# Optimization experiments

Measured on AMD Instinct MI355X. Metric: run time of the kernel, lower is better.

Reference implementation:

```python
import jax, jax.numpy as jnp
import numpy as np

PAD_IDX = 0


def setup_inputs() -> dict:
    key = jax.random.key(0)
    ks = jax.random.split(key, 6)
    nentries, entry_size, bsize, nemb, vocab = 8000, 32, 64, 256, 50000
    keys = jax.random.randint(ks[0], (nentries,), 0, vocab)
    entries = jax.random.randint(ks[1], (nentries, entry_size), 0, vocab)
    query = jax.random.normal(ks[2], (bsize, nemb), dtype=jnp.float32)
    wordemb = jax.random.normal(ks[3], (vocab, nemb), dtype=jnp.float32)
    qproj_w = jax.random.uniform(ks[4], (nemb, nemb), jnp.float32, -0.1, 0.1)
    qproj_b = jnp.zeros((nemb,), jnp.float32)
    return dict(keys=keys, entries=entries, query=query, wordemb=wordemb,
                qproj_w=qproj_w, qproj_b=qproj_b)


def _embed(ids, wordemb):
    # F.embedding with padding_idx: gathered rows at pad_idx are zeroed
    return wordemb[ids] * (ids != PAD_IDX)[..., None].astype(wordemb.dtype)


def reference(keys, entries, query, wordemb, qproj_w, qproj_b):
    keys_e = _embed(keys, wordemb)       # (m, d)
    ents_e = _embed(entries, wordemb)    # (m, n, d)
    # --- single hop (max_hops = 1) ---
    # value_atten: query attends over the n tokens inside each entry
    vq = query @ qproj_w.T + qproj_b                       # (b, d)
    logits_v = jnp.einsum('ik,mnk->imn', vq, ents_e)       # (b, m, n)
    prob_v = jax.nn.softmax(logits_v, axis=-1)
    ents = jnp.einsum('imn,mnk->imk', prob_v, ents_e)      # (b, m, d)
    # entry_atten: query attends over entries via their keys
    logits_e = jnp.einsum('ik,jk->ij', query, keys_e)      # (b, m)
    prob_e = jax.nn.softmax(logits_e, axis=-1)
    o_k = prob_e @ keys_e                                  # (b, d)
    combined = jnp.einsum('bm,bme->be', prob_e, ents)      # (b, d)
    # return (us[-1], prob_list[-1], combined_entries)
    return o_k, logits_e, combined
```

## Files before the change

kernel.cpp:

```cpp
#include <hip/hip_runtime.h>
#include <math.h>

#define B 64
#define D 256
#define M 8000
#define N 32
#define LG_LD 8000
#define EPB 16
#define NBLK (M / EPB)

typedef unsigned short u16;
typedef __bf16 bf16x8 __attribute__((ext_vector_type(8)));
typedef float fx4 __attribute__((ext_vector_type(4)));

#define STR_E  264
#define STR_P  40

static __device__ __forceinline__ u16 f2bf(float x) {
    unsigned int u = __float_as_uint(x);
    u += 0x7FFFu + ((u >> 16) & 1u);
    return (u16)(u >> 16);
}
static __device__ __forceinline__ float bf2f(u16 h) {
    return __uint_as_float(((unsigned)h) << 16);
}
static __device__ __forceinline__ uint4 pack8(float4 va, float4 vb, float msk) {
    unsigned p0 = (unsigned)f2bf(va.x * msk) | ((unsigned)f2bf(va.y * msk) << 16);
    unsigned p1 = (unsigned)f2bf(va.z * msk) | ((unsigned)f2bf(va.w * msk) << 16);
    unsigned p2 = (unsigned)f2bf(vb.x * msk) | ((unsigned)f2bf(vb.y * msk) << 16);
    unsigned p3 = (unsigned)f2bf(vb.z * msk) | ((unsigned)f2bf(vb.w * msk) << 16);
    return make_uint4(p0, p1, p2, p3);
}

__global__ __launch_bounds__(256) void k_prep2(const int* __restrict__ keys,
                                               const float* __restrict__ emb,
                                               const float* __restrict__ q,
                                               const float* __restrict__ W,
                                               const float* __restrict__ bias,
                                               u16* __restrict__ qbf,
                                               u16* __restrict__ keb,
                                               u16* __restrict__ vqb) {
    __shared__ float qs[D];
    int t = threadIdx.x, bid = blockIdx.x;
    if (bid < 1000) {
        int c = bid * 256 + t;
        int j = c >> 5, sp = c & 31;
        int id = keys[j];
        const float* rp = emb + (size_t)id * D + sp * 8;
        float4 v0 = *(const float4*)rp;
        float4 v1 = *(const float4*)(rp + 4);
        float msk = (id != 0) ? 1.f : 0.f;
        uint4 pk = pack8(v0, v1, msk);
        *(uint4*)(keb + (size_t)j * D + sp * 8) = pk;
    } else if (bid < 1008) {
        size_t idx = (size_t)(bid - 1000) * 2048 + (size_t)t * 8;
        float4 v0 = *(const float4*)(q + idx);
        float4 v1 = *(const float4*)(q + idx + 4);
        uint4 pk = pack8(v0, v1, 1.f);
        *(uint4*)(qbf + idx) = pk;
    } else {
        int b = bid - 1008;
        qs[t] = q[b * D + t];
        __syncthreads();
        const float* wr = W + t * D;
        float acc = bias[t];
#pragma unroll 8
        for (int k = 0; k < D; k += 4) {
            float4 w4 = *(const float4*)(wr + k);
            acc += qs[k] * w4.x + qs[k + 1] * w4.y + qs[k + 2] * w4.z + qs[k + 3] * w4.w;
        }
        vqb[b * D + t] = f2bf(acc);
    }
}

__global__ __launch_bounds__(256, 2) void k_heavy_f(const int* __restrict__ entries,
                                                    const float* __restrict__ emb,
                                                    const u16* __restrict__ vqb,
                                                    const u16* __restrict__ qbf,
                                                    const u16* __restrict__ keb,
                                                    float* __restrict__ lg,
                                                    u16* __restrict__ numCp,
                                                    u16* __restrict__ numKp,
                                                    float* __restrict__ mLp,
                                                    float* __restrict__ denLp) {
    __shared__ __align__(16) u16 sEu[2][N * STR_E];
    __shared__ __align__(16) u16 sETu[2][64 * 136];
    __shared__ __align__(16) u16 sPu[B * STR_P];
    __shared__ float sw[EPB][B];

    int t = threadIdx.x;
    int lane = t & 63, l = lane & 15, q = lane >> 4, w = t >> 6;
    int b0 = 16 * w;
    int sp = t & 31, n0 = t >> 5;
    int m0 = blockIdx.x * EPB;
    int bb = t & 63, y = t >> 6;

    int idc[4], idn[4];
    float4 pfF[8];
#pragma unroll
    for (int i = 0; i < 4; ++i) idc[i] = entries[m0 * N + n0 + 8 * i];
#pragma unroll
    for (int i = 0; i < 4; ++i) {
        const float* rp = emb + (size_t)idc[i] * D + sp * 8;
        pfF[2 * i]     = *(const float4*)rp;
        pfF[2 * i + 1] = *(const float4*)(rp + 4);
    }

    fx4 zero4 = {0.f, 0.f, 0.f, 0.f};
    fx4 aL = zero4;
#pragma unroll
    for (int s = 0; s < 8; ++s) {
        bf16x8 a  = *(const bf16x8*)(qbf + (size_t)(b0 + l) * D + 32 * s + 8 * q);
        bf16x8 bq = *(const bf16x8*)(keb + (size_t)(m0 + l) * D + 32 * s + 8 * q);
        aL = __builtin_amdgcn_mfma_f32_16x16x32_bf16(a, bq, aL, 0, 0, 0);
    }
#pragma unroll
    for (int r = 0; r < 4; ++r)
        lg[(size_t)(b0 + 4 * q + r) * LG_LD + m0 + l] = aL[r];

#pragma unroll
    for (int r = 0; r < 4; ++r) {
        float m_ = aL[r];
        m_ = fmaxf(m_, __shfl_xor(m_, 1));
        m_ = fmaxf(m_, __shfl_xor(m_, 2));
        m_ = fmaxf(m_, __shfl_xor(m_, 4));
        m_ = fmaxf(m_, __shfl_xor(m_, 8));
        float wv = __expf(aL[r] - m_);
        sw[l][b0 + 4 * q + r] = wv;
        float d_ = wv;
        d_ += __shfl_xor(d_, 1);
        d_ += __shfl_xor(d_, 2);
        d_ += __shfl_xor(d_, 4);
        d_ += __shfl_xor(d_, 8);
        if (l == 0) {
            mLp[blockIdx.x * B + b0 + 4 * q + r] = m_;
            denLp[blockIdx.x * B + b0 + 4 * q + r] = d_;
        }
    }

    bf16x8 vqf[8];
#pragma unroll
    for (int s = 0; s < 8; ++s)
        vqf[s] = *(const bf16x8*)(vqb + (b0 + l) * D + 32 * s + 8 * q);

    fx4 acc[16];
#pragma unroll
    for (int dt = 0; dt < 16; ++dt) acc[dt] = zero4;

    {
        uint4 pk[4];
#pragma unroll
        for (int i = 0; i < 4; ++i) {
            float msk = (idc[i] != 0) ? 1.f : 0.f;
            pk[i] = pack8(pfF[2 * i], pfF[2 * i + 1], msk);
            *(uint4*)&sEu[0][(n0 + 8 * i) * STR_E + sp * 8] = pk[i];
        }
#pragma unroll
        for (int j = 0; j < 8; ++j) {
            unsigned a0 = (((unsigned*)&pk[0])[j >> 1] >> ((j & 1) * 16)) & 0xFFFFu;
            unsigned a1 = (((unsigned*)&pk[1])[j >> 1] >> ((j & 1) * 16)) & 0xFFFFu;
            unsigned a2 = (((unsigned*)&pk[2])[j >> 1] >> ((j & 1) * 16)) & 0xFFFFu;
            unsigned a3 = (((unsigned*)&pk[3])[j >> 1] >> ((j & 1) * 16)) & 0xFFFFu;
            uint2 pr = make_uint2(a0 | (a1 << 16), a2 | (a3 << 16));
            int off = (2 * sp + (j >> 2)) * 136 + (n0 >> 1) * 32 + (j & 3) * 8 + (n0 & 1) * 4;
            *(uint2*)&sETu[0][off] = pr;
        }
    }
#pragma unroll
    for (int i = 0; i < 4; ++i) idc[i] = entries[(m0 + 1) * N + n0 + 8 * i];
#pragma unroll
    for (int i = 0; i < 4; ++i) {
        const float* rp = emb + (size_t)idc[i] * D + sp * 8;
        pfF[2 * i]     = *(const float4*)rp;
        pfF[2 * i + 1] = *(const float4*)(rp + 4);
    }
#pragma unroll
    for (int i = 0; i < 4; ++i) idn[i] = entries[(m0 + 2) * N + n0 + 8 * i];

    int offL = (l >> 2) * 136 + (l & 3) * 8;

#pragma unroll 2
    for (int e = 0; e < EPB; ++e) {
        __syncthreads();
        int nxt = (e + 1) & 1;
        if (e < EPB - 1) {
            uint4 pk[4];
#pragma unroll
            for (int i = 0; i < 4; ++i) {
                float msk = (idc[i] != 0) ? 1.f : 0.f;
                pk[i] = pack8(pfF[2 * i], pfF[2 * i + 1], msk);
                *(uint4*)&sEu[nxt][(n0 + 8 * i) * STR_E + sp * 8] = pk[i];
            }
#pragma unroll
            for (int j = 0; j < 8; ++j) {
                unsigned a0 = (((unsigned*)&pk[0])[j >> 1] >> ((j & 1) * 16)) & 0xFFFFu;
                unsigned a1 = (((unsigned*)&pk[1])[j >> 1] >> ((j & 1) * 16)) & 0xFFFFu;
                unsigned a2 = (((unsigned*)&pk[2])[j >> 1] >> ((j & 1) * 16)) & 0xFFFFu;
                unsigned a3 = (((unsigned*)&pk[3])[j >> 1] >> ((j & 1) * 16)) & 0xFFFFu;
                uint2 pr = make_uint2(a0 | (a1 << 16), a2 | (a3 << 16));
                int off = (2 * sp + (j >> 2)) * 136 + (n0 >> 1) * 32 + (j & 3) * 8 + (n0 & 1) * 4;
                *(uint2*)&sETu[nxt][off] = pr;
            }
            if (e < EPB - 2) {
#pragma unroll
                for (int i = 0; i < 4; ++i) {
                    const float* rp = emb + (size_t)idn[i] * D + sp * 8;
                    pfF[2 * i]     = *(const float4*)rp;
                    pfF[2 * i + 1] = *(const float4*)(rp + 4);
                }
#pragma unroll
                for (int i = 0; i < 4; ++i) idc[i] = idn[i];
                if (e < EPB - 3) {
#pragma unroll
                    for (int i = 0; i < 4; ++i) idn[i] = entries[(m0 + e + 3) * N + n0 + 8 * i];
                }
            }
        }
        int cur = e & 1;
        fx4 accS[2];
        accS[0] = zero4; accS[1] = zero4;
#pragma unroll
        for (int T = 0; T < 2; ++T)
#pragma unroll
            for (int s = 0; s < 8; ++s) {
                bf16x8 ea = *(const bf16x8*)&sEu[cur][(16 * T + l) * STR_E + 32 * s + 8 * q];
                accS[T] = __builtin_amdgcn_mfma_f32_16x16x32_bf16(ea, vqf[s], accS[T], 0, 0, 0);
            }
        float swb = sw[e][b0 + l];
        float mx = -INFINITY;
#pragma unroll
        for (int T = 0; T < 2; ++T)
#pragma unroll
            for (int r = 0; r < 4; ++r) mx = fmaxf(mx, accS[T][r]);
        mx = fmaxf(mx, __shfl_xor(mx, 16));
        mx = fmaxf(mx, __shfl_xor(mx, 32));
        float pe[2][4], sum = 0.f;
#pragma unroll
        for (int T = 0; T < 2; ++T)
#pragma unroll
            for (int r = 0; r < 4; ++r) {
                pe[T][r] = __expf(accS[T][r] - mx);
                sum += pe[T][r];
            }
        sum += __shfl_xor(sum, 16);
        sum += __shfl_xor(sum, 32);
        float sc = swb / sum;
#pragma unroll
        for (int T = 0; T < 2; ++T)
#pragma unroll
            for (int r = 0; r < 4; ++r) {
                int nn = 16 * T + 4 * q + r;
                int slot = 4 * (nn & 7) + (nn >> 3);
                sPu[(b0 + l) * STR_P + slot] = f2bf(pe[T][r] * sc);
            }
        bf16x8 pa = *(const bf16x8*)&sPu[(b0 + l) * STR_P + 8 * q];
#pragma unroll
        for (int dt = 0; dt < 16; ++dt) {
            bf16x8 eb = *(const bf16x8*)&sETu[cur][offL + dt * 544 + q * 32];
            acc[dt] = __builtin_amdgcn_mfma_f32_16x16x32_bf16(pa, eb, acc[dt], 0, 0, 0);
        }
    }

    u16* ncp = numCp + (size_t)blockIdx.x * (B * D);
#pragma unroll
    for (int dt = 0; dt < 16; ++dt)
#pragma unroll
        for (int r = 0; r < 4; ++r)
            ncp[(b0 + 4 * q + r) * D + 16 * dt + l] = f2bf(acc[dt][r]);

    __syncthreads();
    {
        int rp = t >> 5;
        uint4 ka = *(const uint4*)(keb + (size_t)(m0 + rp) * D + sp * 8);
        uint4 kb = *(const uint4*)(keb + (size_t)(m0 + rp + 8) * D + sp * 8);
#pragma unroll
        for (int j = 0; j < 8; ++j) {
            unsigned a0 = (((unsigned*)&ka)[j >> 1] >> ((j & 1) * 16)) & 0xFFFFu;
            unsigned a1 = (((unsigned*)&kb)[j >> 1] >> ((j & 1) * 16)) & 0xFFFFu;
            int d = 8 * sp + j;
            int sl = 2 * rp;
            int off = (d >> 2) * 136 + (sl >> 3) * 32 + (d & 3) * 8 + (sl & 7);
            *(unsigned*)&sETu[0][off] = a0 | (a1 << 16);
        }
#pragma unroll
        for (int i = 0; i < 4; ++i) {
            int m = 4 * i + y;
            int slot = 2 * (m & 7) + (m >> 3);
            sPu[bb * STR_P + slot] = f2bf(sw[m][bb]);
        }
        *(uint2*)&sPu[bb * STR_P + 16 + 4 * y] = make_uint2(0u, 0u);
    }
    __syncthreads();
    fx4 acc2[16];
#pragma unroll
    for (int dt = 0; dt < 16; ++dt) acc2[dt] = zero4;
    {
        bf16x8 pa2 = *(const bf16x8*)&sPu[(b0 + l) * STR_P + 8 * q];
#pragma unroll
        for (int dt = 0; dt < 16; ++dt) {
            bf16x8 eb2 = *(const bf16x8*)&sETu[0][offL + dt * 544 + q * 32];
            acc2[dt] = __builtin_amdgcn_mfma_f32_16x16x32_bf16(pa2, eb2, acc2[dt], 0, 0, 0);
        }
    }
    u16* nkp = numKp + (size_t)blockIdx.x * (B * D);
#pragma unroll
    for (int dt = 0; dt < 16; ++dt)
#pragma unroll
        for (int r = 0; r < 4; ++r)
            nkp[(b0 + 4 * q + r) * D + 16 * dt + l] = f2bf(acc2[dt][r]);
}

__global__ __launch_bounds__(256) void k_comb2(const u16* __restrict__ numCp,
                                               const u16* __restrict__ numKp,
                                               const float* __restrict__ mLp,
                                               const float* __restrict__ denLp,
                                               float* __restrict__ o_k,
                                               float* __restrict__ comb) {
    __shared__ float sscale[NBLK];
    __shared__ float red[256];
    __shared__ float ro[8][32], rc[8][32];
    __shared__ float srden;
    int bid = blockIdx.x;
    int b = bid >> 3, d0 = (bid & 7) * 32;
    int t = threadIdx.x;
    float mx = -INFINITY;
    for (int blk = t; blk < NBLK; blk += 256) mx = fmaxf(mx, mLp[blk * B + b]);
    red[t] = mx;
    __syncthreads();
    for (int s = 128; s > 0; s >>= 1) {
        if (t < s) red[t] = fmaxf(red[t], red[t + s]);
        __syncthreads();
    }
    float Mg = red[0];
    __syncthreads();
    float ds = 0.f;
    for (int blk = t; blk < NBLK; blk += 256) {
        float sc = __expf(mLp[blk * B + b] - Mg);
        sscale[blk] = sc;
        ds += sc * denLp[blk * B + b];
    }
    red[t] = ds;
    __syncthreads();
    for (int s = 128; s > 0; s >>= 1) {
        if (t < s) red[t] += red[t + s];
        __syncthreads();
    }
    if (t == 0) srden = 1.f / red[0];
    __syncthreads();
    int dd = t & 31, s = t >> 5;
    float ao = 0.f, ac = 0.f;
    for (int blk = s; blk < NBLK; blk += 8) {
        float sc = sscale[blk];
        size_t i = (size_t)blk * (B * D) + (size_t)b * D + d0 + dd;
        ao += sc * bf2f(numKp[i]);
        ac += sc * bf2f(numCp[i]);
    }
    ro[s][dd] = ao;
    rc[s][dd] = ac;
    __syncthreads();
    if (t < 32) {
        float so = 0.f, sc2 = 0.f;
#pragma unroll
        for (int k = 0; k < 8; ++k) { so += ro[k][t]; sc2 += rc[k][t]; }
        float rd = srden;
        o_k[b * D + d0 + t] = so * rd;
        comb[b * D + d0 + t] = sc2 * rd;
    }
}


extern "C" void kernel_launch(void* const* d_in, const int* in_sizes, int n_in,
                              void* d_out, int out_size, void* d_ws, size_t ws_size,
                              hipStream_t stream) {
    const int*   keys    = (const int*)d_in[0];
    const int*   entries = (const int*)d_in[1];
    const float* query   = (const float*)d_in[2];
    const float* wordemb = (const float*)d_in[3];
    const float* qproj_w = (const float*)d_in[4];
    const float* qproj_b = (const float*)d_in[5];

    float* out  = (float*)d_out;
    float* o_k  = out;
    float* lg   = out + B * D;
    float* comb = out + B * D + B * M;

    char* wsb = (char*)d_ws;
    u16*   keb   = (u16*)wsb;
    u16*   qbf   = (u16*)(wsb + 4096000);
    u16*   vqb   = (u16*)(wsb + 4128768);
    u16*   numCp = (u16*)(wsb + 4161536);
    u16*   numKp = (u16*)(wsb + 20545536);
    float* mLp   = (float*)(wsb + 36929536);
    float* denLp = (float*)(wsb + 37057536);

    k_prep2<<<1072, 256, 0, stream>>>(keys, wordemb, query, qproj_w, qproj_b,
                                      qbf, keb, vqb);
    k_heavy_f<<<NBLK, 256, 0, stream>>>(entries, wordemb, vqb, qbf, keb, lg,
                                        numCp, numKp, mLp, denLp);
    k_comb2<<<512, 256, 0, stream>>>(numCp, numKp, mLp, denLp, o_k, comb);
}
```

Measured before the change: 176.3 us.

## Deepen embedding gather prefetch to two entries with ping-pong register buffers

The per-entry loop now keeps two register prefetch buffers (pfA/pfB), so embedding gathers for entry e+2 are issued while entry e is computed. Before, the lookahead was one entry. The __syncthreads calls become a custom barrier that waits only on lgkmcnt, so outstanding global loads no longer stall at each barrier. The softmax-weight shared array is transposed with a padded stride to change its LDS access pattern. The cost is higher register pressure (16 float4 of prefetch state) at 2 blocks per CU, which risks spills or lower occupancy.

```diff
diff --git a/kernel.cpp b/kernel.cpp
--- a/kernel.cpp
+++ b/kernel.cpp
@@ -15,6 +15,7 @@
 
 #define STR_E  264
 #define STR_P  40
+#define STR_W  19
 
 static __device__ __forceinline__ u16 f2bf(float x) {
     unsigned int u = __float_as_uint(x);
@@ -73,6 +74,102 @@
     }
 }
 
+#define BARRIER_LGKM() do {                                   \
+    asm volatile("s_waitcnt lgkmcnt(0)" ::: "memory");        \
+    __builtin_amdgcn_s_barrier();                             \
+    asm volatile("" ::: "memory");                            \
+} while (0)
+
+#define STAGE_BODY(EE, PF, ID) do {                                                     \
+    int nxt_ = (EE) & 1;                                                                \
+    uint4 pk_[4];                                                                       \
+    _Pragma("unroll")                                                                   \
+    for (int i_ = 0; i_ < 4; ++i_) {                                                    \
+        float msk_ = ((ID)[i_] != 0) ? 1.f : 0.f;                                       \
+        pk_[i_] = pack8((PF)[2 * i_], (PF)[2 * i_ + 1], msk_);                          \
+        *(uint4*)&sEu[nxt_][(n0 + 8 * i_) * STR_E + sp * 8] = pk_[i_];                  \
+    }                                                                                   \
+    _Pragma("unroll")                                                                   \
+    for (int j_ = 0; j_ < 8; ++j_) {                                                    \
+        unsigned a0_ = (((unsigned*)&pk_[0])[j_ >> 1] >> ((j_ & 1) * 16)) & 0xFFFFu;    \
+        unsigned a1_ = (((unsigned*)&pk_[1])[j_ >> 1] >> ((j_ & 1) * 16)) & 0xFFFFu;    \
+        unsigned a2_ = (((unsigned*)&pk_[2])[j_ >> 1] >> ((j_ & 1) * 16)) & 0xFFFFu;    \
+        unsigned a3_ = (((unsigned*)&pk_[3])[j_ >> 1] >> ((j_ & 1) * 16)) & 0xFFFFu;    \
+        uint2 pr_ = make_uint2(a0_ | (a1_ << 16), a2_ | (a3_ << 16));                   \
+        int off_ = (2 * sp + (j_ >> 2)) * 136 + (n0 >> 1) * 32 + (j_ & 3) * 8 + (n0 & 1) * 4; \
+        *(uint2*)&sETu[nxt_][off_] = pr_;                                               \
+    }                                                                                   \
+} while (0)
+
+#define COMPUTE_BODY(E) do {                                                            \
+    int cur_ = (E) & 1;                                                                 \
+    fx4 accS_[2];                                                                       \
+    accS_[0] = zero4; accS_[1] = zero4;                                                 \
+    _Pragma("unroll")                                                                   \
+    for (int T_ = 0; T_ < 2; ++T_)                                                      \
+        _Pragma("unroll")                                                               \
+        for (int s_ = 0; s_ < 8; ++s_) {                                                \
+            bf16x8 ea_ = *(const bf16x8*)&sEu[cur_][(16 * T_ + l) * STR_E + 32 * s_ + 8 * q]; \
+            accS_[T_] = __builtin_amdgcn_mfma_f32_16x16x32_bf16(ea_, vqf[s_], accS_[T_], 0, 0, 0); \
+        }                                                                               \
+    float swb_ = swT[b0 + l][(E)];                                                      \
+    float mx_ = -INFINITY;                                                              \
+    _Pragma("unroll")                                                                   \
+    for (int T_ = 0; T_ < 2; ++T_)                                                      \
+        _Pragma("unroll")                                                               \
+        for (int r_ = 0; r_ < 4; ++r_) mx_ = fmaxf(mx_, accS_[T_][r_]);                 \
+    mx_ = fmaxf(mx_, __shfl_xor(mx_, 16));                                              \
+    mx_ = fmaxf(mx_, __shfl_xor(mx_, 32));                                              \
+    float pe_[2][4], sum_ = 0.f;                                                        \
+    _Pragma("unroll")                                                                   \
+    for (int T_ = 0; T_ < 2; ++T_)                                                      \
+        _Pragma("unroll")                                                               \
+        for (int r_ = 0; r_ < 4; ++r_) {                                                \
+            pe_[T_][r_] = __expf(accS_[T_][r_] - mx_);                                  \
+            sum_ += pe_[T_][r_];                                                        \
+        }                                                                               \
+    sum_ += __shfl_xor(sum_, 16);                                                       \
+    sum_ += __shfl_xor(sum_, 32);                                                       \
+    float sc_ = swb_ / sum_;                                                            \
+    _Pragma("unroll")                                                                   \
+    for (int T_ = 0; T_ < 2; ++T_)                                                      \
+        _Pragma("unroll")                                                               \
+        for (int r_ = 0; r_ < 4; ++r_) {                                                \
+            int nn_ = 16 * T_ + 4 * q + r_;                                             \
+            int slot_ = 4 * (nn_ & 7) + (nn_ >> 3);                                     \
+            sPu[(b0 + l) * STR_P + slot_] = f2bf(pe_[T_][r_] * sc_);                    \
+        }                                                                               \
+    bf16x8 pa_ = *(const bf16x8*)&sPu[(b0 + l) * STR_P + 8 * q];                        \
+    _Pragma("unroll")                                                                   \
+    for (int dt_ = 0; dt_ < 16; ++dt_) {                                                \
+        bf16x8 eb_ = *(const bf16x8*)&sETu[cur_][offL + dt_ * 544 + q * 32];            \
+        acc[dt_] = __builtin_amdgcn_mfma_f32_16x16x32_bf16(pa_, eb_, acc[dt_], 0, 0, 0); \
+    }                                                                                   \
+} while (0)
+
+#define ITER(E, PF, ID) do {                                                            \
+    BARRIER_LGKM();                                                                     \
+    if ((E) < EPB - 1) {                                                                \
+        STAGE_BODY((E) + 1, PF, ID);                                                    \
+        if ((E) < EPB - 3) {                                                            \
+            _Pragma("unroll")                                                           \
+            for (int i_ = 0; i_ < 4; ++i_) (ID)[i_] = idn[i_];                          \
+            _Pragma("unroll")                                                           \
+            for (int i_ = 0; i_ < 4; ++i_) {                                            \
+                const float* rp_ = emb + (size_t)(ID)[i_] * D + sp * 8;                 \
+                (PF)[2 * i_]     = *(const float4*)rp_;                                 \
+                (PF)[2 * i_ + 1] = *(const float4*)(rp_ + 4);                           \
+            }                                                                           \
+            if ((E) < EPB - 4) {                                                        \
+                _Pragma("unroll")                                                       \
+                for (int i_ = 0; i_ < 4; ++i_)                                          \
+                    idn[i_] = entries[(m0 + (E) + 4) * N + n0 + 8 * i_];                \
+            }                                                                           \
+        }                                                                               \
+    }                                                                                   \
+    COMPUTE_BODY(E);                                                                    \
+} while (0)
+
 __global__ __launch_bounds__(256, 2) void k_heavy_f(const int* __restrict__ entries,
                                                     const float* __restrict__ emb,
                                                     const u16* __restrict__ vqb,
@@ -86,7 +183,7 @@
     __shared__ __align__(16) u16 sEu[2][N * STR_E];
     __shared__ __align__(16) u16 sETu[2][64 * 136];
     __shared__ __align__(16) u16 sPu[B * STR_P];
-    __shared__ float sw[EPB][B];
+    __shared__ float swT[B][STR_W];
 
     int t = threadIdx.x;
     int lane = t & 63, l = lane & 15, q = lane >> 4, w = t >> 6;
@@ -95,15 +192,16 @@
     int m0 = blockIdx.x * EPB;
     int bb = t & 63, y = t >> 6;
 
-    int idc[4], idn[4];
-    float4 pfF[8];
-#pragma unroll
-    for (int i = 0; i < 4; ++i) idc[i] = entries[m0 * N + n0 + 8 * i];
+    float4 pfA[8], pfB[8];
+    int idA[4], idB[4], idn[4];
+
+#pragma unroll
+    for (int i = 0; i < 4; ++i) idB[i] = entries[m0 * N + n0 + 8 * i];
 #pragma unroll
     for (int i = 0; i < 4; ++i) {
-        const float* rp = emb + (size_t)idc[i] * D + sp * 8;
-        pfF[2 * i]     = *(const float4*)rp;
-        pfF[2 * i + 1] = *(const float4*)(rp + 4);
+        const float* rp = emb + (size_t)idB[i] * D + sp * 8;
+        pfB[2 * i]     = *(const float4*)rp;
+        pfB[2 * i + 1] = *(const float4*)(rp + 4);
     }
 
     fx4 zero4 = {0.f, 0.f, 0.f, 0.f};
@@ -126,7 +224,7 @@
         m_ = fmaxf(m_, __shfl_xor(m_, 4));
         m_ = fmaxf(m_, __shfl_xor(m_, 8));
         float wv = __expf(aL[r] - m_);
-        sw[l][b0 + 4 * q + r] = wv;
+        swT[b0 + 4 * q + r][l] = wv;
         float d_ = wv;
         d_ += __shfl_xor(d_, 1);
         d_ += __shfl_xor(d_, 2);
@@ -147,118 +245,31 @@
 #pragma unroll
     for (int dt = 0; dt < 16; ++dt) acc[dt] = zero4;
 
-    {
-        uint4 pk[4];
-#pragma unroll
-        for (int i = 0; i < 4; ++i) {
-            float msk = (idc[i] != 0) ? 1.f : 0.f;
-            pk[i] = pack8(pfF[2 * i], pfF[2 * i + 1], msk);
-            *(uint4*)&sEu[0][(n0 + 8 * i) * STR_E + sp * 8] = pk[i];
-        }
-#pragma unroll
-        for (int j = 0; j < 8; ++j) {
-            unsigned a0 = (((unsigned*)&pk[0])[j >> 1] >> ((j & 1) * 16)) & 0xFFFFu;
-            unsigned a1 = (((unsigned*)&pk[1])[j >> 1] >> ((j & 1) * 16)) & 0xFFFFu;
-            unsigned a2 = (((unsigned*)&pk[2])[j >> 1] >> ((j & 1) * 16)) & 0xFFFFu;
-            unsigned a3 = (((unsigned*)&pk[3])[j >> 1] >> ((j & 1) * 16)) & 0xFFFFu;
-            uint2 pr = make_uint2(a0 | (a1 << 16), a2 | (a3 << 16));
-            int off = (2 * sp + (j >> 2)) * 136 + (n0 >> 1) * 32 + (j & 3) * 8 + (n0 & 1) * 4;
-            *(uint2*)&sETu[0][off] = pr;
-        }
-    }
-#pragma unroll
-    for (int i = 0; i < 4; ++i) idc[i] = entries[(m0 + 1) * N + n0 + 8 * i];
+    int offL = (l >> 2) * 136 + (l & 3) * 8;
+
+    STAGE_BODY(0, pfB, idB);
+#pragma unroll
+    for (int i = 0; i < 4; ++i) idB[i] = entries[(m0 + 1) * N + n0 + 8 * i];
 #pragma unroll
     for (int i = 0; i < 4; ++i) {
-        const float* rp = emb + (size_t)idc[i] * D + sp * 8;
-        pfF[2 * i]     = *(const float4*)rp;
-        pfF[2 * i + 1] = *(const float4*)(rp + 4);
-    }
-#pragma unroll
-    for (int i = 0; i < 4; ++i) idn[i] = entries[(m0 + 2) * N + n0 + 8 * i];
-
-    int offL = (l >> 2) * 136 + (l & 3) * 8;
-
-#pragma unroll 2
-    for (int e = 0; e < EPB; ++e) {
-        __syncthreads();
-        int nxt = (e + 1) & 1;
-        if (e < EPB - 1) {
-            uint4 pk[4];
-#pragma unroll
-            for (int i = 0; i < 4; ++i) {
-                float msk = (idc[i] != 0) ? 1.f : 0.f;
-                pk[i] = pack8(pfF[2 * i], pfF[2 * i + 1], msk);
-                *(uint4*)&sEu[nxt][(n0 + 8 * i) * STR_E + sp * 8] = pk[i];
-            }
-#pragma unroll
-            for (int j = 0; j < 8; ++j) {
-                unsigned a0 = (((unsigned*)&pk[0])[j >> 1] >> ((j & 1) * 16)) & 0xFFFFu;
-                unsigned a1 = (((unsigned*)&pk[1])[j >> 1] >> ((j & 1) * 16)) & 0xFFFFu;
-                unsigned a2 = (((unsigned*)&pk[2])[j >> 1] >> ((j & 1) * 16)) & 0xFFFFu;
-                unsigned a3 = (((unsigned*)&pk[3])[j >> 1] >> ((j & 1) * 16)) & 0xFFFFu;
-                uint2 pr = make_uint2(a0 | (a1 << 16), a2 | (a3 << 16));
-                int off = (2 * sp + (j >> 2)) * 136 + (n0 >> 1) * 32 + (j & 3) * 8 + (n0 & 1) * 4;
-                *(uint2*)&sETu[nxt][off] = pr;
-            }
-            if (e < EPB - 2) {
-#pragma unroll
-                for (int i = 0; i < 4; ++i) {
-                    const float* rp = emb + (size_t)idn[i] * D + sp * 8;
-                    pfF[2 * i]     = *(const float4*)rp;
-                    pfF[2 * i + 1] = *(const float4*)(rp + 4);
-                }
-#pragma unroll
-                for (int i = 0; i < 4; ++i) idc[i] = idn[i];
-                if (e < EPB - 3) {
-#pragma unroll
-                    for (int i = 0; i < 4; ++i) idn[i] = entries[(m0 + e + 3) * N + n0 + 8 * i];
-                }
-            }
-        }
-        int cur = e & 1;
-        fx4 accS[2];
-        accS[0] = zero4; accS[1] = zero4;
-#pragma unroll
-        for (int T = 0; T < 2; ++T)
-#pragma unroll
-            for (int s = 0; s < 8; ++s) {
-                bf16x8 ea = *(const bf16x8*)&sEu[cur][(16 * T + l) * STR_E + 32 * s + 8 * q];
-                accS[T] = __builtin_amdgcn_mfma_f32_16x16x32_bf16(ea, vqf[s], accS[T], 0, 0, 0);
-            }
-        float swb = sw[e][b0 + l];
-        float mx = -INFINITY;
-#pragma unroll
-        for (int T = 0; T < 2; ++T)
-#pragma unroll
-            for (int r = 0; r < 4; ++r) mx = fmaxf(mx, accS[T][r]);
-        mx = fmaxf(mx, __shfl_xor(mx, 16));
-        mx = fmaxf(mx, __shfl_xor(mx, 32));
-        float pe[2][4], sum = 0.f;
-#pragma unroll
-        for (int T = 0; T < 2; ++T)
-#pragma unroll
-            for (int r = 0; r < 4; ++r) {
-                pe[T][r] = __expf(accS[T][r] - mx);
-                sum += pe[T][r];
-            }
-        sum += __shfl_xor(sum, 16);
-        sum += __shfl_xor(sum, 32);
-        float sc = swb / sum;
-#pragma unroll
-        for (int T = 0; T < 2; ++T)
-#pragma unroll
-            for (int r = 0; r < 4; ++r) {
-                int nn = 16 * T + 4 * q + r;
-                int slot = 4 * (nn & 7) + (nn >> 3);
-                sPu[(b0 + l) * STR_P + slot] = f2bf(pe[T][r] * sc);
-            }
-        bf16x8 pa = *(const bf16x8*)&sPu[(b0 + l) * STR_P + 8 * q];
-#pragma unroll
-        for (int dt = 0; dt < 16; ++dt) {
-            bf16x8 eb = *(const bf16x8*)&sETu[cur][offL + dt * 544 + q * 32];
-            acc[dt] = __builtin_amdgcn_mfma_f32_16x16x32_bf16(pa, eb, acc[dt], 0, 0, 0);
-        }
+        const float* rp = emb + (size_t)idB[i] * D + sp * 8;
+        pfB[2 * i]     = *(const float4*)rp;
+        pfB[2 * i + 1] = *(const float4*)(rp + 4);
+    }
+#pragma unroll
+    for (int i = 0; i < 4; ++i) idA[i] = entries[(m0 + 2) * N + n0 + 8 * i];
+#pragma unroll
+    for (int i = 0; i < 4; ++i) {
+        const float* rp = emb + (size_t)idA[i] * D + sp * 8;
+        pfA[2 * i]     = *(const float4*)rp;
+        pfA[2 * i + 1] = *(const float4*)(rp + 4);
+    }
+#pragma unroll
+    for (int i = 0; i < 4; ++i) idn[i] = entries[(m0 + 3) * N + n0 + 8 * i];
+
+    for (int e = 0; e < EPB; e += 2) {
+        ITER(e, pfB, idB);
+        ITER(e + 1, pfA, idA);
     }
 
     u16* ncp = numCp + (size_t)blockIdx.x * (B * D);
@@ -268,7 +279,7 @@
         for (int r = 0; r < 4; ++r)
             ncp[(b0 + 4 * q + r) * D + 16 * dt + l] = f2bf(acc[dt][r]);
 
-    __syncthreads();
+    BARRIER_LGKM();
     {
         int rp = t >> 5;
         uint4 ka = *(const uint4*)(keb + (size_t)(m0 + rp) * D + sp * 8);
@@ -286,11 +297,11 @@
         for (int i = 0; i < 4; ++i) {
             int m = 4 * i + y;
             int slot = 2 * (m & 7) + (m >> 3);
-            sPu[bb * STR_P + slot] = f2bf(sw[m][bb]);
+            sPu[bb * STR_P + slot] = f2bf(swT[bb][m]);
         }
         *(uint2*)&sPu[bb * STR_P + 16 + 4 * y] = make_uint2(0u, 0u);
     }
-    __syncthreads();
+    BARRIER_LGKM();
     fx4 acc2[16];
 #pragma unroll
     for (int dt = 0; dt < 16; ++dt) acc2[dt] = zero4;
@@ -309,6 +320,10 @@
         for (int r = 0; r < 4; ++r)
             nkp[(b0 + 4 * q + r) * D + 16 * dt + l] = f2bf(acc2[dt][r]);
 }
+
+#undef ITER
+#undef COMPUTE_BODY
+#undef STAGE_BODY
 
 __global__ __launch_bounds__(256) void k_comb2(const u16* __restrict__ numCp,
                                                const u16* __restrict__ numKp,
```

Result: no change. 177.8 us (+0.9%).
